# Performance work log

Measured on AMD Instinct MI355X. Metric: run time of the kernel, lower is better.

The kernel has to match this reference:

```python
import jax, jax.numpy as jnp
import numpy as np

N = 100_000      # nodes
E = 1_600_000    # edges (avg degree 16)
FIN = 128
FOUT = 64
C = 1.0          # Poincare ball curvature (args.c)
T = 0.48         # threshold (forward default)
MIN_NORM = 1e-15
PROJ_EPS = 4e-3  # float32 boundary eps used by standard PoincareBall.proj


def _artanh(x):
    x = jnp.clip(x, -1.0 + 1e-7, 1.0 - 1e-7)
    return 0.5 * (jnp.log1p(x) - jnp.log1p(-x))


def logmap0(p, c):
    sc = c ** 0.5
    n = jnp.clip(jnp.linalg.norm(p, axis=-1, keepdims=True), MIN_NORM, None)
    return p / (sc * n) * _artanh(sc * n)


def expmap0(u, c):
    sc = c ** 0.5
    n = jnp.clip(jnp.linalg.norm(u, axis=-1, keepdims=True), MIN_NORM, None)
    return jnp.tanh(sc * n) * u / (sc * n)


def proj(x, c):
    n = jnp.clip(jnp.linalg.norm(x, axis=-1, keepdims=True), MIN_NORM, None)
    maxn = (1.0 - PROJ_EPS) / (c ** 0.5)
    return jnp.where(n > maxn, x / n * maxn, x)


def setup_inputs() -> dict:
    key = jax.random.key(0)
    k0, k1, k2, k3, k4 = jax.random.split(key, 5)
    # points near the origin of the Poincare ball
    x = jax.random.normal(k0, (N, FIN), dtype=jnp.float32) * 0.05
    edge_index = jax.random.randint(k1, (2, E), 0, N, dtype=jnp.int32)
    W_up = jax.random.normal(k2, (FIN, FOUT), dtype=jnp.float32) / np.float32(np.sqrt(FIN))
    W_pl = jax.random.normal(k3, (FOUT, 2), dtype=jnp.float32) / np.float32(np.sqrt(FOUT))
    W_lw = jax.random.normal(k4, (2 * FOUT, 1), dtype=jnp.float32) / np.float32(np.sqrt(2 * FOUT))
    return {"x": x, "edge_index": edge_index, "W_up": W_up, "W_pl": W_pl, "W_lw": W_lw}


def reference(x, edge_index, W_up, W_pl, W_lw):
    src, dst = edge_index[0], edge_index[1]

    def agg(v):  # PyG add-aggregation: out[i] = sum_{(j->i)} v[j]
        return jax.ops.segment_sum(v[src], dst, num_segments=N)

    x_tan = logmap0(x, C)                                   # [N, FIN]
    updated_x = jax.nn.leaky_relu(x_tan @ W_up)             # [N, FOUT], slope 0.01
    sum_neigh = agg(updated_x)                              # [N, FOUT]
    random_prob = jax.nn.softmax(jax.nn.relu(sum_neigh @ W_pl), axis=-1)  # [N, 2]
    sel_v = jnp.where(random_prob[:, 1:2] > T, 1.0, 0.0)    # [N, 1] hard gate
    sum_sel = agg(sel_v * updated_x)                        # [N, FOUT]
    weight_sel = jax.nn.sigmoid(jnp.concatenate([sum_sel, sum_neigh], axis=-1) @ W_lw)  # [N, 1]
    a_x = jax.nn.relu(agg(weight_sel * sel_v * updated_x))  # [N, FOUT]
    out = updated_x + a_x
    return proj(expmap0(out, C), C)
```

## Files before the change

kernel.cpp:

```cpp
#include <hip/hip_runtime.h>
#include <math.h>

#define FIN 128
#define FOUT 64
#define MAXDEG 64
#define BKT_SHIFT 7
#define BKT_CAP 2560


__device__ __forceinline__ float4 f4add(float4 a, float4 b) {
  return make_float4(a.x + b.x, a.y + b.y, a.z + b.z, a.w + b.w);
}
__device__ __forceinline__ float4 f4fma(float c, float4 v, float4 a) {
  return make_float4(fmaf(c, v.x, a.x), fmaf(c, v.y, a.y),
                     fmaf(c, v.z, a.z), fmaf(c, v.w, a.w));
}
__device__ __forceinline__ float4 f4shflxor(float4 v, int off) {
  return make_float4(__shfl_xor(v.x, off, 64), __shfl_xor(v.y, off, 64),
                     __shfl_xor(v.z, off, 64), __shfl_xor(v.w, off, 64));
}
__device__ __forceinline__ float red16(float v) {
  v += __shfl_xor(v, 1, 64);
  v += __shfl_xor(v, 2, 64);
  v += __shfl_xor(v, 4, 64);
  v += __shfl_xor(v, 8, 64);
  return v;
}
__device__ __forceinline__ float wave_sum(float v) {
#pragma unroll
  for (int off = 1; off <= 32; off <<= 1) v += __shfl_xor(v, off, 64);
  return v;
}

__device__ __forceinline__ float row_scale(float ss) {
  float n  = sqrtf(ss);
  float nc = fmaxf(n, 1e-15f);
  float t  = fminf(nc, 1.0f - 1e-7f);
  float at = 0.5f * (log1pf(t) - log1pf(-t));
  return at / nc;
}

__device__ __forceinline__ float leaky(float v) {
  return (v >= 0.f) ? v : 0.01f * v;
}

__device__ __forceinline__ unsigned int bf16rne(float x) {
  unsigned int b = __float_as_uint(x);
  b += 0x7FFFu + ((b >> 16) & 1u);
  return b >> 16;
}
__device__ __forceinline__ float4 bf4(uint2 v) {
  return make_float4(__uint_as_float(v.x << 16),
                     __uint_as_float(v.x & 0xFFFF0000u),
                     __uint_as_float(v.y << 16),
                     __uint_as_float(v.y & 0xFFFF0000u));
}

__global__ __launch_bounds__(256) void k_main(const float* __restrict__ x,
                                              const float* __restrict__ Wup,
                                              const float* __restrict__ Wpl,
                                              const float* __restrict__ Wlw,
                                              float* __restrict__ u,
                                              float* __restrict__ scl4,
                                              const int* __restrict__ ei, int E,
                                              int nb, int* __restrict__ bcnt,
                                              int2* __restrict__ stg,
                                              int N, int gemmBlocks) {
  __shared__ float buf[8192];
  __shared__ float wls[256];
  __shared__ float ps[256];
  __shared__ float scl[64];

  int t = threadIdx.x;

  if (blockIdx.x >= gemmBlocks) {
    int* hist = (int*)buf;
    int* base = hist + nb;
    int bb = blockIdx.x - gemmBlocks;
    for (int h = t; h < nb; h += 256) hist[h] = 0;
    __syncthreads();
    int e0 = bb * 4096 + t * 16;
    int sv[16], dv[16];
#pragma unroll
    for (int j = 0; j < 16; j += 4) {
      int e = e0 + j;
      if (e + 3 < E) {
        int4 s4 = *(const int4*)(ei + e);
        int4 d4 = *(const int4*)(ei + E + e);
        sv[j] = s4.x; sv[j+1] = s4.y; sv[j+2] = s4.z; sv[j+3] = s4.w;
        dv[j] = d4.x; dv[j+1] = d4.y; dv[j+2] = d4.z; dv[j+3] = d4.w;
      } else {
        for (int q = 0; q < 4; ++q) {
          int ee = e + q;
          sv[j+q] = (ee < E) ? ei[ee] : -1;
          dv[j+q] = (ee < E) ? ei[E + ee] : -1;
        }
      }
    }
#pragma unroll
    for (int j = 0; j < 16; ++j)
      if (dv[j] >= 0) atomicAdd(&hist[dv[j] >> BKT_SHIFT], 1);
    __syncthreads();
    for (int h = t; h < nb; h += 256)
      base[h] = hist[h] ? atomicAdd(&bcnt[h], hist[h]) : 0;
    __syncthreads();
    for (int h = t; h < nb; h += 256) hist[h] = 0;
    __syncthreads();
#pragma unroll
    for (int j = 0; j < 16; ++j) {
      if (dv[j] < 0) continue;
      int b = dv[j] >> BKT_SHIFT;
      int p = base[b] + atomicAdd(&hist[b], 1);
      if (p < BKT_CAP) stg[(size_t)b * BKT_CAP + p] = make_int2(sv[j], dv[j]);
    }
    return;
  }

  int n0 = blockIdx.x * 64;
  {
    int proj = t >> 6, f = t & 63;
    float wv = (proj == 0) ? Wpl[f * 2]
             : (proj == 1) ? Wpl[f * 2 + 1]
             : (proj == 2) ? Wlw[f] : Wlw[64 + f];
    wls[t] = wv;
  }

  {
    int n  = t & 63;
    int kq = t >> 6;
    int gn = n0 + n;
    bool ok = gn < N;
    const float4* xr = (const float4*)(x + (size_t)gn * FIN);
    float ssum = 0.f;
    float4 r0[8];
#pragma unroll
    for (int m = 0; m < 8; ++m)
      r0[m] = ok ? xr[kq * 8 + m] : make_float4(0.f, 0.f, 0.f, 0.f);
#pragma unroll
    for (int m = 0; m < 8; ++m) {
      float4 v = r0[m];
      ssum = fmaf(v.x, v.x, fmaf(v.y, v.y, fmaf(v.z, v.z, fmaf(v.w, v.w, ssum))));
      int kf = kq * 32 + m * 4;
      buf[(kf + 0) * 64 + n] = v.x;
      buf[(kf + 1) * 64 + n] = v.y;
      buf[(kf + 2) * 64 + n] = v.z;
      buf[(kf + 3) * 64 + n] = v.w;
    }
    ps[t] = ssum;
  }
  __syncthreads();
  if (t < 64) scl[t] = row_scale(ps[t] + ps[t + 64] + ps[t + 128] + ps[t + 192]);

  int wave = t >> 6, lane = t & 63;
  int j = lane & 3, i = lane >> 2;
  const float* xp = buf + i * 4;
  const float* wg = Wup + wave * 16 + j * 4;
  float4 a0 = make_float4(0,0,0,0), a1 = a0, a2 = a0, a3 = a0;
#pragma unroll 8
  for (int k = 0; k < FIN; ++k) {
    float4 xv = *(const float4*)(xp + k * 64);
    float4 wv = *(const float4*)(wg + k * 64);
    a0 = f4fma(xv.x, wv, a0);
    a1 = f4fma(xv.y, wv, a1);
    a2 = f4fma(xv.z, wv, a2);
    a3 = f4fma(xv.w, wv, a3);
  }
  __syncthreads();

  int fbase = wave * 16 + j * 4;
#pragma unroll
  for (int r = 0; r < 4; ++r) {
    float4 acc = (r == 0) ? a0 : (r == 1) ? a1 : (r == 2) ? a2 : a3;
    int nn = i * 4 + r;
    int gnn = n0 + nn;
    float sc = scl[nn];
    float4 o = make_float4(leaky(sc * acc.x), leaky(sc * acc.y),
                           leaky(sc * acc.z), leaky(sc * acc.w));
    if (gnn < N) *(float4*)(u + (size_t)gnn * FOUT + fbase) = o;
    buf[nn * 67 + fbase]     = o.x;
    buf[nn * 67 + fbase + 1] = o.y;
    buf[nn * 67 + fbase + 2] = o.z;
    buf[nn * 67 + fbase + 3] = o.w;
  }
  __syncthreads();

  {
    int proj = t >> 6;
    const float* wc = wls + proj * 64;
    int nn = t & 63;
    int gnn = n0 + nn;
    const float* ur = buf + nn * 67;
    float acc = 0.f;
#pragma unroll 8
    for (int f = 0; f < 64; ++f) acc = fmaf(ur[f], wc[f], acc);
    if (gnn < N) scl4[(size_t)gnn * 4 + proj] = acc;
  }
}

__global__ __launch_bounds__(256) void k_binB(const int2* __restrict__ stg,
                                              const int* __restrict__ bcnt,
                                              int N, int* __restrict__ deg,
                                              int* __restrict__ slots) {
  __shared__ int cur[128];
  int b = blockIdx.x, t = threadIdx.x;
  if (t < 128) cur[t] = 0;
  __syncthreads();
  int cnt = min(bcnt[b], BKT_CAP);
  int dbase = b << BKT_SHIFT;
  const int2* sp = stg + (size_t)b * BKT_CAP;
  for (int i = t; i < cnt; i += 256) {
    int2 e = sp[i];
    int p = atomicAdd(&cur[e.y - dbase], 1);
    if (p < MAXDEG) slots[(size_t)e.y * MAXDEG + p] = e.x;
  }
  __syncthreads();
  if (t < 128) {
    int dst = dbase + t;
    if (dst < N) {
      int c = min(cur[t], MAXDEG);
      deg[dst] = c;
      int cr = (c + 15) & ~15;
      for (int p = c; p < cr; ++p) slots[(size_t)dst * MAXDEG + p] = N;
    }
  }
}

__global__ __launch_bounds__(256) void k_aggA(const int* __restrict__ deg,
                                              const int* __restrict__ slots,
                                              const float4* __restrict__ scl4,
                                              float* __restrict__ selF,
                                              float* __restrict__ gq,
                                              float* __restrict__ tp, int N) {
  int wv = threadIdx.x >> 6, lane = threadIdx.x & 63;
  int g = lane >> 4, l16 = lane & 15;
  int i = blockIdx.x * 16 + wv * 4 + g;
  bool act = (i < N);
  int d = act ? deg[i] : 0;
  float ax = 0.f, ay = 0.f, aw = 0.f;
#pragma unroll
  for (int q = 0; q < 4; ++q) {
    int k = l16 + q * 16;
    if (k < d) {
      int s = slots[(size_t)i * MAXDEG + k];
      float4 gg = scl4[s];
      ax += gg.x; ay += gg.y; aw += gg.w;
    }
  }
  ax = red16(ax); ay = red16(ay); aw = red16(aw);
  if (act && l16 == 0) {
    float r0 = fmaxf(ax, 0.f), r1 = fmaxf(ay, 0.f);
    float m  = fmaxf(r0, r1);
    float e0 = expf(r0 - m), e1 = expf(r1 - m);
    float p  = e1 / (e0 + e1);
    float sel = (p > 0.48f) ? 1.f : 0.f;
    float4 own = scl4[i];
    selF[i] = sel;
    gq[i]   = sel * own.z;
    tp[i]   = aw;
  }
}

__global__ __launch_bounds__(256) void k_aggB(const int* __restrict__ deg,
                                              const int* __restrict__ slots,
                                              const float* __restrict__ gq,
                                              const float* __restrict__ tp,
                                              const float* __restrict__ selF,
                                              const float* __restrict__ u,
                                              unsigned int* __restrict__ uw,
                                              int N) {
  if (blockIdx.x == 0 && threadIdx.x < 32)
    uw[(size_t)N * 32 + threadIdx.x] = 0u;
  int wv = threadIdx.x >> 6, lane = threadIdx.x & 63;
  int i = blockIdx.x * 4 + wv;
  if (i >= N) return;
  int d = deg[i];
  bool valid = lane < d;
  int s = 0;
  if (valid) s = slots[(size_t)i * MAXDEG + lane];
  float v = gq[s];
  float t = tp[i] + wave_sum(valid ? v : 0.f);
  float seli = selF[i];
  float val = 0.f;
  if (seli != 0.f) {
    float sig = 1.f / (1.f + expf(-t));
    val = sig * u[(size_t)i * 64 + lane];
  }
  unsigned int b = bf16rne(val);
  unsigned int partner = (unsigned int)__shfl_xor((int)b, 1, 64);
  if ((lane & 1) == 0)
    uw[(size_t)i * 32 + (lane >> 1)] = (b & 0xFFFFu) | (partner << 16);
}

__global__ __launch_bounds__(256) void k_agg3(const int* __restrict__ deg,
                                              const int* __restrict__ slots,
                                              const float* __restrict__ selF,
                                              const float* __restrict__ u,
                                              const uint2* __restrict__ uw,
                                              float* __restrict__ out, int N) {
  __shared__ int comp[4][64];
  int wv = threadIdx.x >> 6, lane = threadIdx.x & 63;
  int i = blockIdx.x * 4 + wv;
  if (i >= N) return;
  int d = deg[i];
  bool valid = lane < d;
  int s = 0;
  if (valid) s = slots[(size_t)i * MAXDEG + lane];
  bool flag = valid && (selF[s] != 0.f);
  unsigned long long mask = __ballot(flag);
  int cnt = __popcll(mask);
  comp[wv][lane] = N;
  int rank = __popcll(mask & ((1ull << lane) - 1ull));
  if (flag) comp[wv][rank] = s;
  int sub = lane >> 4, l4 = lane & 15;
  float4 acc0 = make_float4(0, 0, 0, 0), acc1 = acc0;
  for (int k0 = 0; k0 < cnt; k0 += 8) {
    int s0 = comp[wv][k0 + sub];
    int s1 = comp[wv][k0 + sub + 4];
    uint2 w0 = uw[(size_t)s0 * 16 + l4];
    uint2 w1 = uw[(size_t)s1 * 16 + l4];
    acc0 = f4add(acc0, bf4(w0));
    acc1 = f4add(acc1, bf4(w1));
  }
  float4 acc = f4add(acc0, acc1);
  acc = f4add(acc, f4shflxor(acc, 16));
  acc = f4add(acc, f4shflxor(acc, 32));
  float4 uv = ((const float4*)(u + (size_t)i * 64))[l4];
  float4 ov = make_float4(uv.x + fmaxf(acc.x, 0.f), uv.y + fmaxf(acc.y, 0.f),
                          uv.z + fmaxf(acc.z, 0.f), uv.w + fmaxf(acc.w, 0.f));
  float ssp = ov.x * ov.x + ov.y * ov.y + ov.z * ov.z + ov.w * ov.w;
  float ss  = red16(ssp);
  float nc  = fmaxf(sqrtf(ss), 1e-15f);
  float th  = tanhf(nc);
  float fac = th / nc;
  float4 r = make_float4(ov.x * fac, ov.y * fac, ov.z * fac, ov.w * fac);
  float n2 = fmaxf(th, 1e-15f);
  float maxn = 1.0f - 4e-3f;
  float sc = (n2 > maxn) ? (maxn / n2) : 1.0f;
  float4 res = make_float4(r.x * sc, r.y * sc, r.z * sc, r.w * sc);
  if (sub == 0) ((float4*)(out + (size_t)i * 64))[l4] = res;
}

extern "C" void kernel_launch(void* const* d_in, const int* in_sizes, int n_in,
                              void* d_out, int out_size, void* d_ws, size_t ws_size,
                              hipStream_t stream) {
  const float* x   = (const float*)d_in[0];
  const int*   ei  = (const int*)d_in[1];
  const float* Wup = (const float*)d_in[2];
  const float* Wpl = (const float*)d_in[3];
  const float* Wlw = (const float*)d_in[4];
  float* out = (float*)d_out;

  int N = in_sizes[0] / FIN;
  int E = in_sizes[1] / 2;
  int nb = (N + (1 << BKT_SHIFT) - 1) >> BKT_SHIFT;

  char* ws = (char*)d_ws;
  float* u     = (float*)ws;
  int*   slots = (int*)(u + (size_t)N * 64);
  char*  regB  = (char*)(slots + (size_t)N * MAXDEG);
  size_t regB_sz = (size_t)nb * BKT_CAP * sizeof(int2);
  int2*  stg   = (int2*)regB;
  unsigned int* uwp = (unsigned int*)regB;
  float* scl4  = (float*)(regB + regB_sz);
  int*   deg   = (int*)(scl4 + (size_t)N * 4);
  float* selF  = (float*)(deg + N);
  float* gq    = selF + N;
  float* tp    = gq + N;
  int*   bcnt  = (int*)(tp + N);

  hipMemsetAsync(bcnt, 0, nb * sizeof(int), stream);

  int gemmBlocks = (N + 63) / 64;
  int binABlocks = (E + 4095) / 4096;
  k_main<<<gemmBlocks + binABlocks, 256, 0, stream>>>(
      x, Wup, Wpl, Wlw, u, scl4, ei, E, nb, bcnt, stg, N, gemmBlocks);
  k_binB<<<nb, 256, 0, stream>>>(stg, bcnt, N, deg, slots);
  k_aggA<<<(N + 15) / 16, 256, 0, stream>>>(deg, slots, (const float4*)scl4, selF, gq, tp, N);
  int nblk = (N + 3) / 4;
  k_aggB<<<nblk, 256, 0, stream>>>(deg, slots, gq, tp, selF, u, uwp, N);
  k_agg3<<<nblk, 256, 0, stream>>>(deg, slots, selF, u, (const uint2*)uwp, out, N);
}
```

Measured before the change: 232.0 us.

## Build adjacency directly with global atomics and drop bf16 weighted-feature staging

Replaces the two-pass bucketed edge binning (block histogram, staging buffer, separate binB kernel) with direct per-destination global atomic slot insertion inside the fused main kernel, after a memset of the degree array. The per-node weighted bf16 copy of features is removed. A small kernel now computes a scalar sigmoid weight per node, and the final aggregation gathers fp32 rows of u scaled by that weight. This removes one kernel launch and the staging and bf16 write traffic, at the cost of heavily contended scattered global atomics and doubled gather bytes in the final aggregation. Neighbor order in slots becomes nondeterministic, and padding slots are no longer written.

```diff
diff --git a/kernel.cpp b/kernel.cpp
--- a/kernel.cpp
+++ b/kernel.cpp
@@ -4,8 +4,6 @@
 #define FIN 128
 #define FOUT 64
 #define MAXDEG 64
-#define BKT_SHIFT 7
-#define BKT_CAP 2560
 
 
 __device__ __forceinline__ float4 f4add(float4 a, float4 b) {
@@ -26,11 +24,6 @@
   v += __shfl_xor(v, 8, 64);
   return v;
 }
-__device__ __forceinline__ float wave_sum(float v) {
-#pragma unroll
-  for (int off = 1; off <= 32; off <<= 1) v += __shfl_xor(v, off, 64);
-  return v;
-}
 
 __device__ __forceinline__ float row_scale(float ss) {
   float n  = sqrtf(ss);
@@ -42,18 +35,6 @@
 
 __device__ __forceinline__ float leaky(float v) {
   return (v >= 0.f) ? v : 0.01f * v;
-}
-
-__device__ __forceinline__ unsigned int bf16rne(float x) {
-  unsigned int b = __float_as_uint(x);
-  b += 0x7FFFu + ((b >> 16) & 1u);
-  return b >> 16;
-}
-__device__ __forceinline__ float4 bf4(uint2 v) {
-  return make_float4(__uint_as_float(v.x << 16),
-                     __uint_as_float(v.x & 0xFFFF0000u),
-                     __uint_as_float(v.y << 16),
-                     __uint_as_float(v.y & 0xFFFF0000u));
 }
 
 __global__ __launch_bounds__(256) void k_main(const float* __restrict__ x,
@@ -63,8 +44,8 @@
                                               float* __restrict__ u,
                                               float* __restrict__ scl4,
                                               const int* __restrict__ ei, int E,
-                                              int nb, int* __restrict__ bcnt,
-                                              int2* __restrict__ stg,
+                                              int* __restrict__ deg,
+                                              int* __restrict__ slots,
                                               int N, int gemmBlocks) {
   __shared__ float buf[8192];
   __shared__ float wls[256];
@@ -74,44 +55,32 @@
   int t = threadIdx.x;
 
   if (blockIdx.x >= gemmBlocks) {
-    int* hist = (int*)buf;
-    int* base = hist + nb;
     int bb = blockIdx.x - gemmBlocks;
-    for (int h = t; h < nb; h += 256) hist[h] = 0;
-    __syncthreads();
     int e0 = bb * 4096 + t * 16;
-    int sv[16], dv[16];
 #pragma unroll
     for (int j = 0; j < 16; j += 4) {
       int e = e0 + j;
       if (e + 3 < E) {
         int4 s4 = *(const int4*)(ei + e);
         int4 d4 = *(const int4*)(ei + E + e);
-        sv[j] = s4.x; sv[j+1] = s4.y; sv[j+2] = s4.z; sv[j+3] = s4.w;
-        dv[j] = d4.x; dv[j+1] = d4.y; dv[j+2] = d4.z; dv[j+3] = d4.w;
+        int p0 = atomicAdd(&deg[d4.x], 1);
+        if (p0 < MAXDEG) slots[(size_t)d4.x * MAXDEG + p0] = s4.x;
+        int p1 = atomicAdd(&deg[d4.y], 1);
+        if (p1 < MAXDEG) slots[(size_t)d4.y * MAXDEG + p1] = s4.y;
+        int p2 = atomicAdd(&deg[d4.z], 1);
+        if (p2 < MAXDEG) slots[(size_t)d4.z * MAXDEG + p2] = s4.z;
+        int p3 = atomicAdd(&deg[d4.w], 1);
+        if (p3 < MAXDEG) slots[(size_t)d4.w * MAXDEG + p3] = s4.w;
       } else {
         for (int q = 0; q < 4; ++q) {
           int ee = e + q;
-          sv[j+q] = (ee < E) ? ei[ee] : -1;
-          dv[j+q] = (ee < E) ? ei[E + ee] : -1;
+          if (ee < E) {
+            int sv = ei[ee], dv = ei[E + ee];
+            int p = atomicAdd(&deg[dv], 1);
+            if (p < MAXDEG) slots[(size_t)dv * MAXDEG + p] = sv;
+          }
         }
       }
-    }
-#pragma unroll
-    for (int j = 0; j < 16; ++j)
-      if (dv[j] >= 0) atomicAdd(&hist[dv[j] >> BKT_SHIFT], 1);
-    __syncthreads();
-    for (int h = t; h < nb; h += 256)
-      base[h] = hist[h] ? atomicAdd(&bcnt[h], hist[h]) : 0;
-    __syncthreads();
-    for (int h = t; h < nb; h += 256) hist[h] = 0;
-    __syncthreads();
-#pragma unroll
-    for (int j = 0; j < 16; ++j) {
-      if (dv[j] < 0) continue;
-      int b = dv[j] >> BKT_SHIFT;
-      int p = base[b] + atomicAdd(&hist[b], 1);
-      if (p < BKT_CAP) stg[(size_t)b * BKT_CAP + p] = make_int2(sv[j], dv[j]);
     }
     return;
   }
@@ -197,34 +166,6 @@
   }
 }
 
-__global__ __launch_bounds__(256) void k_binB(const int2* __restrict__ stg,
-                                              const int* __restrict__ bcnt,
-                                              int N, int* __restrict__ deg,
-                                              int* __restrict__ slots) {
-  __shared__ int cur[128];
-  int b = blockIdx.x, t = threadIdx.x;
-  if (t < 128) cur[t] = 0;
-  __syncthreads();
-  int cnt = min(bcnt[b], BKT_CAP);
-  int dbase = b << BKT_SHIFT;
-  const int2* sp = stg + (size_t)b * BKT_CAP;
-  for (int i = t; i < cnt; i += 256) {
-    int2 e = sp[i];
-    int p = atomicAdd(&cur[e.y - dbase], 1);
-    if (p < MAXDEG) slots[(size_t)e.y * MAXDEG + p] = e.x;
-  }
-  __syncthreads();
-  if (t < 128) {
-    int dst = dbase + t;
-    if (dst < N) {
-      int c = min(cur[t], MAXDEG);
-      deg[dst] = c;
-      int cr = (c + 15) & ~15;
-      for (int p = c; p < cr; ++p) slots[(size_t)dst * MAXDEG + p] = N;
-    }
-  }
-}
-
 __global__ __launch_bounds__(256) void k_aggA(const int* __restrict__ deg,
                                               const int* __restrict__ slots,
                                               const float4* __restrict__ scl4,
@@ -235,7 +176,7 @@
   int g = lane >> 4, l16 = lane & 15;
   int i = blockIdx.x * 16 + wv * 4 + g;
   bool act = (i < N);
-  int d = act ? deg[i] : 0;
+  int d = act ? min(deg[i], MAXDEG) : 0;
   float ax = 0.f, ay = 0.f, aw = 0.f;
 #pragma unroll
   for (int q = 0; q < 4; ++q) {
@@ -260,66 +201,65 @@
   }
 }
 
-__global__ __launch_bounds__(256) void k_aggB(const int* __restrict__ deg,
+__global__ __launch_bounds__(256) void k_wgt(const int* __restrict__ deg,
+                                             const int* __restrict__ slots,
+                                             const float* __restrict__ gq,
+                                             const float* __restrict__ tp,
+                                             const float* __restrict__ selF,
+                                             float* __restrict__ ws, int N) {
+  int wv = threadIdx.x >> 6, lane = threadIdx.x & 63;
+  int g = lane >> 4, l16 = lane & 15;
+  int i = blockIdx.x * 16 + wv * 4 + g;
+  bool act = (i < N);
+  int d = act ? min(deg[i], MAXDEG) : 0;
+  float a = 0.f;
+#pragma unroll
+  for (int q = 0; q < 4; ++q) {
+    int k = l16 + q * 16;
+    if (k < d) {
+      int s = slots[(size_t)i * MAXDEG + k];
+      a += gq[s];
+    }
+  }
+  a = red16(a);
+  if (act && l16 == 0) {
+    float tt = tp[i] + a;
+    float w = (selF[i] != 0.f) ? 1.f / (1.f + expf(-tt)) : 0.f;
+    ws[i] = w;
+  }
+}
+
+__global__ __launch_bounds__(256) void k_agg3(const int* __restrict__ deg,
                                               const int* __restrict__ slots,
-                                              const float* __restrict__ gq,
-                                              const float* __restrict__ tp,
-                                              const float* __restrict__ selF,
+                                              const float* __restrict__ ws,
                                               const float* __restrict__ u,
-                                              unsigned int* __restrict__ uw,
-                                              int N) {
-  if (blockIdx.x == 0 && threadIdx.x < 32)
-    uw[(size_t)N * 32 + threadIdx.x] = 0u;
+                                              float* __restrict__ out, int N) {
+  __shared__ int comp[4][64];
+  __shared__ float wsc[4][64];
   int wv = threadIdx.x >> 6, lane = threadIdx.x & 63;
   int i = blockIdx.x * 4 + wv;
   if (i >= N) return;
-  int d = deg[i];
+  int d = min(deg[i], MAXDEG);
   bool valid = lane < d;
   int s = 0;
   if (valid) s = slots[(size_t)i * MAXDEG + lane];
-  float v = gq[s];
-  float t = tp[i] + wave_sum(valid ? v : 0.f);
-  float seli = selF[i];
-  float val = 0.f;
-  if (seli != 0.f) {
-    float sig = 1.f / (1.f + expf(-t));
-    val = sig * u[(size_t)i * 64 + lane];
-  }
-  unsigned int b = bf16rne(val);
-  unsigned int partner = (unsigned int)__shfl_xor((int)b, 1, 64);
-  if ((lane & 1) == 0)
-    uw[(size_t)i * 32 + (lane >> 1)] = (b & 0xFFFFu) | (partner << 16);
-}
-
-__global__ __launch_bounds__(256) void k_agg3(const int* __restrict__ deg,
-                                              const int* __restrict__ slots,
-                                              const float* __restrict__ selF,
-                                              const float* __restrict__ u,
-                                              const uint2* __restrict__ uw,
-                                              float* __restrict__ out, int N) {
-  __shared__ int comp[4][64];
-  int wv = threadIdx.x >> 6, lane = threadIdx.x & 63;
-  int i = blockIdx.x * 4 + wv;
-  if (i >= N) return;
-  int d = deg[i];
-  bool valid = lane < d;
-  int s = 0;
-  if (valid) s = slots[(size_t)i * MAXDEG + lane];
-  bool flag = valid && (selF[s] != 0.f);
+  float w = valid ? ws[s] : 0.f;
+  bool flag = w > 0.f;
   unsigned long long mask = __ballot(flag);
   int cnt = __popcll(mask);
-  comp[wv][lane] = N;
+  comp[wv][lane] = 0;
+  wsc[wv][lane]  = 0.f;
   int rank = __popcll(mask & ((1ull << lane) - 1ull));
-  if (flag) comp[wv][rank] = s;
+  if (flag) { comp[wv][rank] = s; wsc[wv][rank] = w; }
   int sub = lane >> 4, l4 = lane & 15;
   float4 acc0 = make_float4(0, 0, 0, 0), acc1 = acc0;
   for (int k0 = 0; k0 < cnt; k0 += 8) {
-    int s0 = comp[wv][k0 + sub];
-    int s1 = comp[wv][k0 + sub + 4];
-    uint2 w0 = uw[(size_t)s0 * 16 + l4];
-    uint2 w1 = uw[(size_t)s1 * 16 + l4];
-    acc0 = f4add(acc0, bf4(w0));
-    acc1 = f4add(acc1, bf4(w1));
+    int s0 = comp[wv][k0 + sub];     float w0 = wsc[wv][k0 + sub];
+    int s1 = comp[wv][k0 + sub + 4]; float w1 = wsc[wv][k0 + sub + 4];
+    float4 u0 = ((const float4*)(u + (size_t)s0 * 64))[l4];
+    float4 u1 = ((const float4*)(u + (size_t)s1 * 64))[l4];
+    acc0 = f4fma(w0, u0, acc0);
+    acc1 = f4fma(w1, u1, acc1);
   }
   float4 acc = f4add(acc0, acc1);
   acc = f4add(acc, f4shflxor(acc, 16));
@@ -352,31 +292,25 @@
 
   int N = in_sizes[0] / FIN;
   int E = in_sizes[1] / 2;
-  int nb = (N + (1 << BKT_SHIFT) - 1) >> BKT_SHIFT;
-
-  char* ws = (char*)d_ws;
-  float* u     = (float*)ws;
+
+  char* ws_p = (char*)d_ws;
+  float* u     = (float*)ws_p;
   int*   slots = (int*)(u + (size_t)N * 64);
-  char*  regB  = (char*)(slots + (size_t)N * MAXDEG);
-  size_t regB_sz = (size_t)nb * BKT_CAP * sizeof(int2);
-  int2*  stg   = (int2*)regB;
-  unsigned int* uwp = (unsigned int*)regB;
-  float* scl4  = (float*)(regB + regB_sz);
+  float* scl4  = (float*)(slots + (size_t)N * MAXDEG);
   int*   deg   = (int*)(scl4 + (size_t)N * 4);
   float* selF  = (float*)(deg + N);
   float* gq    = selF + N;
   float* tp    = gq + N;
-  int*   bcnt  = (int*)(tp + N);
-
-  hipMemsetAsync(bcnt, 0, nb * sizeof(int), stream);
+  float* ws    = tp + N;
+
+  hipMemsetAsync(deg, 0, N * sizeof(int), stream);
 
   int gemmBlocks = (N + 63) / 64;
-  int binABlocks = (E + 4095) / 4096;
-  k_main<<<gemmBlocks + binABlocks, 256, 0, stream>>>(
-      x, Wup, Wpl, Wlw, u, scl4, ei, E, nb, bcnt, stg, N, gemmBlocks);
-  k_binB<<<nb, 256, 0, stream>>>(stg, bcnt, N, deg, slots);
-  k_aggA<<<(N + 15) / 16, 256, 0, stream>>>(deg, slots, (const float4*)scl4, selF, gq, tp, N);
-  int nblk = (N + 3) / 4;
-  k_aggB<<<nblk, 256, 0, stream>>>(deg, slots, gq, tp, selF, u, uwp, N);
-  k_agg3<<<nblk, 256, 0, stream>>>(deg, slots, selF, u, (const uint2*)uwp, out, N);
-}
+  int csrBlocks  = (E + 4095) / 4096;
+  k_main<<<gemmBlocks + csrBlocks, 256, 0, stream>>>(
+      x, Wup, Wpl, Wlw, u, scl4, ei, E, deg, slots, N, gemmBlocks);
+  int nblk16 = (N + 15) / 16;
+  k_aggA<<<nblk16, 256, 0, stream>>>(deg, slots, (const float4*)scl4, selF, gq, tp, N);
+  k_wgt<<<nblk16, 256, 0, stream>>>(deg, slots, gq, tp, selF, ws, N);
+  k_agg3<<<(N + 3) / 4, 256, 0, stream>>>(deg, slots, ws, u, out, N);
+}
```

New measurement: 273.0 us. +17.7%, slower.
